# Performance work log

Hardware: AMD Instinct MI355X
Metric: run time of the kernel (lower is better)

The kernel has to match this reference:

```python
import jax, jax.numpy as jnp
import numpy as np

B, LQ, LK, E, H = 2, 1024, 10000, 256, 8
D = E // H  # head_dim = 32


def setup_inputs() -> dict:
    key = jax.random.key(0)
    ks = jax.random.split(key, 10)
    s = 1.0 / np.sqrt(E).astype(np.float32)
    return {
        "bev_emb": jax.random.normal(ks[0], (B, LK, E), jnp.float32),
        "queries": jax.random.normal(ks[1], (B, LQ, E), jnp.float32),
        "Wq": jax.random.normal(ks[2], (E, E), jnp.float32) * s,
        "bq": jax.random.normal(ks[3], (E,), jnp.float32) * 0.01,
        "Wk": jax.random.normal(ks[4], (E, E), jnp.float32) * s,
        "bk": jax.random.normal(ks[5], (E,), jnp.float32) * 0.01,
        "Wv": jax.random.normal(ks[6], (E, E), jnp.float32) * s,
        "bv": jax.random.normal(ks[7], (E,), jnp.float32) * 0.01,
        "Wo": jax.random.normal(ks[8], (E, E), jnp.float32) * s,
        "bo": jax.random.normal(ks[9], (E,), jnp.float32) * 0.01,
    }


def reference(bev_emb, queries, Wq, bq, Wk, bk, Wv, bv, Wo, bo):
    Bn, Lq, Em = queries.shape
    Lk = bev_emb.shape[1]
    q = (queries @ Wq + bq).reshape(Bn, Lq, H, D)
    k = (bev_emb @ Wk + bk).reshape(Bn, Lk, H, D)
    v = (bev_emb @ Wv + bv).reshape(Bn, Lk, H, D)
    # NOTE: source applies no 1/sqrt(head_dim) scaling
    energy = jnp.einsum('bqhd,bkhd->bhqk', q, k)  # [B,H,Lq,Lk]
    attn = jax.nn.softmax(energy, axis=-1)
    out = jnp.einsum('bhqk,bkhd->bqhd', attn, v).reshape(Bn, Lq, Em)
    return out @ Wo + bo
```

## Files before the change

### kernel.cpp

```cpp
#include <hip/hip_runtime.h>
#include <hip/hip_bf16.h>

#define B_  2
#define LQ_ 1024
#define LK_ 10000
#define E_  256
#define H_  8
#define D_  32
#define NT_ ((LK_ + 63) / 64)

typedef __attribute__((ext_vector_type(8))) short bf16x8;
typedef __attribute__((ext_vector_type(4))) short bf16x4;
typedef __attribute__((ext_vector_type(4))) float f32x4;

#define LOG2E 1.4426950408889634f

static __device__ __forceinline__ short bfc(float x) {
  __bf16 b = (__bf16)x;
  return __builtin_bit_cast(short, b);
}
static __device__ __forceinline__ float bf2f(short s) {
  return (float)__builtin_bit_cast(__bf16, s);
}

#if __has_builtin(__builtin_amdgcn_exp2f)
static __device__ __forceinline__ float ex2(float x) {
  return __builtin_amdgcn_exp2f(x);
}
#else
static __device__ __forceinline__ float ex2(float x) { return exp2f(x); }
#endif

#if __has_builtin(__builtin_amdgcn_mfma_f32_16x16x16bf16_1k)
static __device__ __forceinline__ f32x4 mfma_pv(bf16x4 a, bf16x4 b, f32x4 c) {
  return __builtin_amdgcn_mfma_f32_16x16x16bf16_1k(a, b, c, 0, 0, 0);
}
#else
static __device__ __forceinline__ f32x4 mfma_pv(bf16x4 a, bf16x4 b, f32x4 c) {
  asm volatile("s_nop 1\n\tv_mfma_f32_16x16x16_bf16 %0, %1, %2, %0"
               : "+v"(c) : "v"(a), "v"(b));
  return c;
}
#endif

static __device__ __forceinline__ int xcd_swizzle(int flat, int nwg) {
  const int xcd = flat & 7, rest = flat >> 3;
  const int q = nwg >> 3, r = nwg & 7;
  return (xcd < r ? xcd * (q + 1) : r * (q + 1) + (xcd - r) * q) + rest;
}

static __device__ __forceinline__ void split8(const float4& a, const float4& b,
                                              bf16x8& hi, bf16x8& lo) {
  float v[8] = {a.x, a.y, a.z, a.w, b.x, b.y, b.z, b.w};
#pragma unroll
  for (int i = 0; i < 8; ++i) {
    const short h = bfc(v[i]);
    hi[i] = h;
    lo[i] = bfc(v[i] - bf2f(h));
  }
}

__global__ __launch_bounds__(256) void wtrans4(
    const float* __restrict__ W0, const float* __restrict__ W1,
    const float* __restrict__ W2, const float* __restrict__ W3,
    unsigned short* __restrict__ T0, unsigned short* __restrict__ T1,
    unsigned short* __restrict__ T2, unsigned short* __restrict__ T3) {
  const float* W;
  unsigned short* T;
  switch (blockIdx.z) {
    case 0:  W = W0; T = T0; break;
    case 1:  W = W1; T = T1; break;
    case 2:  W = W2; T = T2; break;
    default: W = W3; T = T3; break;
  }
  __shared__ float ts[16][17];
  const int tx = threadIdx.x & 15;
  const int ty = threadIdx.x >> 4;
  const int k0 = blockIdx.x * 16;
  const int n0 = blockIdx.y * 16;
  ts[ty][tx] = W[(size_t)(k0 + ty) * 256 + n0 + tx];
  __syncthreads();
  T[(size_t)(n0 + ty) * 256 + k0 + tx] = (unsigned short)bfc(ts[tx][ty]);
}

template <bool KV, bool F32OUT>
__global__ __launch_bounds__(256) void proj_wave(
    const float* __restrict__ A,
    const unsigned short* __restrict__ Wt1,
    const unsigned short* __restrict__ Wt2,
    const float* __restrict__ b1, const float* __restrict__ b2,
    void* __restrict__ C1v, void* __restrict__ C2v) {
  const int lane = threadIdx.x & 63;
  const int nt   = threadIdx.x >> 6;
  const int mt   = blockIdx.x;
  const int lr   = lane & 15;
  const int oc   = lane >> 4;
  const int m0   = mt * 32;
  const int n0   = nt * 64;

  f32x4 ac1[2][4];
  f32x4 ac2[2][4];
#pragma unroll
  for (int s = 0; s < 2; ++s)
#pragma unroll
    for (int q = 0; q < 4; ++q) {
      ac1[s][q] = (f32x4){0.f, 0.f, 0.f, 0.f};
      if (KV) ac2[s][q] = (f32x4){0.f, 0.f, 0.f, 0.f};
    }

  const float* a0p = &A[(size_t)(m0 + lr) * 256 + oc * 8];
  const float* a1p = a0p + 16 * 256;

  float4 c0a = *(const float4*)(a0p + 0);
  float4 c0b = *(const float4*)(a0p + 4);
  float4 c1a = *(const float4*)(a1p + 0);
  float4 c1b = *(const float4*)(a1p + 4);

  for (int kb = 0; kb < 8; ++kb) {
    bf16x8 ah0, al0, ah1, al1;
    split8(c0a, c0b, ah0, al0);
    split8(c1a, c1b, ah1, al1);

    const size_t wko = (size_t)(kb * 32 + oc * 8);
    bf16x8 w1[4], w2[4];
#pragma unroll
    for (int q = 0; q < 4; ++q) {
      w1[q] = *(const bf16x8*)&Wt1[(size_t)(n0 + q * 16 + lr) * 256 + wko];
      if (KV) w2[q] = *(const bf16x8*)&Wt2[(size_t)(n0 + q * 16 + lr) * 256 + wko];
    }

    if (kb < 7) {
      c0a = *(const float4*)(a0p + (kb + 1) * 32 + 0);
      c0b = *(const float4*)(a0p + (kb + 1) * 32 + 4);
      c1a = *(const float4*)(a1p + (kb + 1) * 32 + 0);
      c1b = *(const float4*)(a1p + (kb + 1) * 32 + 4);
    }

#pragma unroll
    for (int q = 0; q < 4; ++q) {
      ac1[0][q] = __builtin_amdgcn_mfma_f32_16x16x32_bf16(w1[q], ah0, ac1[0][q], 0, 0, 0);
      ac1[0][q] = __builtin_amdgcn_mfma_f32_16x16x32_bf16(w1[q], al0, ac1[0][q], 0, 0, 0);
      ac1[1][q] = __builtin_amdgcn_mfma_f32_16x16x32_bf16(w1[q], ah1, ac1[1][q], 0, 0, 0);
      ac1[1][q] = __builtin_amdgcn_mfma_f32_16x16x32_bf16(w1[q], al1, ac1[1][q], 0, 0, 0);
      if (KV) {
        ac2[0][q] = __builtin_amdgcn_mfma_f32_16x16x32_bf16(w2[q], ah0, ac2[0][q], 0, 0, 0);
        ac2[1][q] = __builtin_amdgcn_mfma_f32_16x16x32_bf16(w2[q], ah1, ac2[1][q], 0, 0, 0);
      }
    }
  }

#pragma unroll
  for (int s = 0; s < 2; ++s) {
#pragma unroll
    for (int q = 0; q < 4; ++q) {
      const int m = m0 + s * 16 + lr;
      const int n = n0 + q * 16 + oc * 4;
      const float4 bv1 = *(const float4*)&b1[n];
      if (F32OUT) {
        float4 o;
        o.x = ac1[s][q][0] + bv1.x; o.y = ac1[s][q][1] + bv1.y;
        o.z = ac1[s][q][2] + bv1.z; o.w = ac1[s][q][3] + bv1.w;
        *(float4*)&((float*)C1v)[(size_t)m * 256 + n] = o;
      } else {
        ushort4 o;
        o.x = (unsigned short)bfc(ac1[s][q][0] + bv1.x);
        o.y = (unsigned short)bfc(ac1[s][q][1] + bv1.y);
        o.z = (unsigned short)bfc(ac1[s][q][2] + bv1.z);
        o.w = (unsigned short)bfc(ac1[s][q][3] + bv1.w);
        *(ushort4*)&((unsigned short*)C1v)[(size_t)m * 256 + n] = o;
      }
      if (KV) {
        const float4 bv2 = *(const float4*)&b2[n];
        ushort4 o;
        o.x = (unsigned short)bfc(ac2[s][q][0] + bv2.x);
        o.y = (unsigned short)bfc(ac2[s][q][1] + bv2.y);
        o.z = (unsigned short)bfc(ac2[s][q][2] + bv2.z);
        o.w = (unsigned short)bfc(ac2[s][q][3] + bv2.w);
        *(ushort4*)&((unsigned short*)C2v)[(size_t)m * 256 + n] = o;
      }
    }
  }
}

__global__ __launch_bounds__(256) void attn_mfma(const float* __restrict__ q,
                                                 const unsigned short* __restrict__ kbf,
                                                 const unsigned short* __restrict__ vbf,
                                                 float* __restrict__ Opart,
                                                 float* __restrict__ lpart,
                                                 float* __restrict__ o_direct,
                                                 int tiles_per_split, int nsplit) {
  const int nwg = 128 * gridDim.z;
  const int l   = xcd_swizzle(blockIdx.x + 16 * (blockIdx.y + 8 * blockIdx.z), nwg);
  const int qb   = l & 15;
  const int h    = (l >> 4) & 7;
  const int z    = l >> 7;
  const int s_id = z / B_;
  const int b    = z % B_;
  const int t    = threadIdx.x;
  const int lane = t & 63;
  const int w    = t >> 6;
  const int lq   = lane & 15;
  const int grp  = lane >> 4;

  __shared__ ushort Klds[2][64][64];
  __shared__ ushort Vtld[2][32][64];

  const int t0 = s_id * tiles_per_split;
  const int t1 = min(NT_, t0 + tiles_per_split);

  const int qrow = qb * 64 + w * 16 + lq;
  bf16x8 qfrag;
  {
    const float* qp = &q[((size_t)(b * LQ_ + qrow)) * E_ + h * D_ + grp * 8];
    const float4 q0 = *(const float4*)qp;
    const float4 q1 = *(const float4*)(qp + 4);
    qfrag[0] = bfc(q0.x * LOG2E); qfrag[1] = bfc(q0.y * LOG2E);
    qfrag[2] = bfc(q0.z * LOG2E); qfrag[3] = bfc(q0.w * LOG2E);
    qfrag[4] = bfc(q1.x * LOG2E); qfrag[5] = bfc(q1.y * LOG2E);
    qfrag[6] = bfc(q1.z * LOG2E); qfrag[7] = bfc(q1.w * LOG2E);
  }

  const int krow_l = t >> 2;
  const int kchunk = t & 3;
  const int vkp    = t >> 3;
  const int vd     = (t & 7) * 4;

  float l_run = 0.f;
  f32x4 acc0 = {0.f, 0.f, 0.f, 0.f};
  f32x4 acc1 = {0.f, 0.f, 0.f, 0.f};

  const size_t kvrow0 = (size_t)b * LK_;

  uint4 kval; ushort4 v0, v1;
  auto load_tile = [&](int kn) {
    if (kn == NT_ - 1) {
      const int krow  = min(kn * 64 + krow_l, LK_ - 1);
      const int vrow0 = min(kn * 64 + 2 * vkp, LK_ - 1);
      const int vrow1 = min(kn * 64 + 2 * vkp + 1, LK_ - 1);
      kval = *(const uint4*)&kbf[(kvrow0 + krow) * E_ + h * D_ + kchunk * 8];
      v0 = *(const ushort4*)&vbf[(kvrow0 + vrow0) * E_ + h * D_ + vd];
      v1 = *(const ushort4*)&vbf[(kvrow0 + vrow1) * E_ + h * D_ + vd];
    } else {
      kval = *(const uint4*)&kbf[(kvrow0 + kn * 64 + krow_l) * E_ + h * D_ + kchunk * 8];
      v0 = *(const ushort4*)&vbf[(kvrow0 + kn * 64 + 2 * vkp) * E_ + h * D_ + vd];
      v1 = *(const ushort4*)&vbf[(kvrow0 + kn * 64 + 2 * vkp + 1) * E_ + h * D_ + vd];
    }
  };
  auto store_tile = [&](int buf) {
    *(uint4*)((char*)&Klds[buf][krow_l][0] + ((kchunk * 16) ^ ((krow_l & 7) << 4))) = kval;
#pragma unroll
    for (int i = 0; i < 4; ++i) {
      const int d = vd + i;
      *(ushort2*)((char*)&Vtld[buf][d][0] + ((vkp * 4) ^ ((d & 7) << 4))) =
          make_ushort2(((const unsigned short*)&v0)[i], ((const unsigned short*)&v1)[i]);
    }
  };

  load_tile(t0);
  store_tile(0);
  if (t0 + 1 < t1) load_tile(t0 + 1);
  __syncthreads();

  int cur = 0;
  for (int kt = t0; kt < t1; ++kt) {
    const int rem = LK_ - kt * 64;

    if (kt + 1 < t1) store_tile(cur ^ 1);
    if (kt + 2 < t1) load_tile(kt + 2);

    f32x4 p[4];
    __builtin_amdgcn_s_setprio(1);
#pragma unroll
    for (int s = 0; s < 4; ++s) {
      const int row = s * 16 + lq;
      const bf16x8 kf = *(const bf16x8*)((const char*)&Klds[cur][row][0] +
                                         ((grp * 16) ^ ((row & 7) << 4)));
      const f32x4 zero = {0.f, 0.f, 0.f, 0.f};
      p[s] = __builtin_amdgcn_mfma_f32_16x16x32_bf16(kf, qfrag, zero, 0, 0, 0);
    }
    __builtin_amdgcn_s_setprio(0);

    bf16x4 pb[4];
    if (rem >= 64) {
#pragma unroll
      for (int s = 0; s < 4; ++s)
#pragma unroll
        for (int r = 0; r < 4; ++r) {
          const float e = ex2(p[s][r]);
          l_run += e;
          pb[s][r] = bfc(e);
        }
    } else {
#pragma unroll
      for (int s = 0; s < 4; ++s) {
        const bool vs = (s * 16 + grp * 4) < rem;
#pragma unroll
        for (int r = 0; r < 4; ++r) {
          const float e = vs ? ex2(p[s][r]) : 0.f;
          l_run += e;
          pb[s][r] = bfc(e);
        }
      }
    }

    __builtin_amdgcn_s_setprio(1);
#pragma unroll
    for (int s = 0; s < 4; ++s) {
      {
        const int row = lq;
        const bf16x4 vf = *(const bf16x4*)((const char*)&Vtld[cur][row][0] +
                                           ((s * 32 + grp * 8) ^ ((row & 7) << 4)));
        acc0 = mfma_pv(vf, pb[s], acc0);
      }
      {
        const int row = 16 + lq;
        const bf16x4 vf = *(const bf16x4*)((const char*)&Vtld[cur][row][0] +
                                           ((s * 32 + grp * 8) ^ ((row & 7) << 4)));
        acc1 = mfma_pv(vf, pb[s], acc1);
      }
    }
    __builtin_amdgcn_s_setprio(0);

    __syncthreads();
    cur ^= 1;
  }

  l_run += __shfl_xor(l_run, 16);
  l_run += __shfl_xor(l_run, 32);

  if (nsplit == 1) {
    const float inv = 1.f / l_run;
    float* op = &o_direct[((size_t)(b * LQ_ + qrow)) * E_ + h * D_];
#pragma unroll
    for (int r = 0; r < 4; ++r) {
      op[grp * 4 + r]      = acc0[r] * inv;
      op[16 + grp * 4 + r] = acc1[r] * inv;
    }
  } else {
    const size_t pbase =
        (size_t)s_id * (B_ * H_ * LQ_) + ((size_t)b * H_ + h) * LQ_ + qrow;
#pragma unroll
    for (int r = 0; r < 4; ++r) {
      Opart[pbase * D_ + grp * 4 + r]      = acc0[r];
      Opart[pbase * D_ + 16 + grp * 4 + r] = acc1[r];
    }
    if (grp == 0) lpart[pbase] = l_run;
  }
}

__global__ __launch_bounds__(256) void attn_merge(const float* __restrict__ Opart,
                                                  const float* __restrict__ lpart,
                                                  float* __restrict__ o, int S) {
  const int idx = blockIdx.x * 256 + threadIdx.x;
  if (idx >= B_ * LQ_ * E_) return;
  const int e   = idx & (E_ - 1);
  const int row = idx >> 8;
  const int b   = row >> 10;
  const int qq  = row & (LQ_ - 1);
  const int h   = e >> 5;
  const int d   = e & (D_ - 1);
  const size_t base   = ((size_t)b * H_ + h) * LQ_ + qq;
  const size_t stride = (size_t)B_ * H_ * LQ_;

  float lsum = 0.f, osum = 0.f;
  for (int s = 0; s < S; ++s) {
    lsum += lpart[s * stride + base];
    osum += Opart[(s * stride + base) * D_ + d];
  }
  o[idx] = osum / lsum;
}

extern "C" void kernel_launch(void* const* d_in, const int* in_sizes, int n_in,
                              void* d_out, int out_size, void* d_ws, size_t ws_size,
                              hipStream_t stream) {
  const float* bev     = (const float*)d_in[0];
  const float* queries = (const float*)d_in[1];
  const float* Wq      = (const float*)d_in[2];
  const float* bq      = (const float*)d_in[3];
  const float* Wk      = (const float*)d_in[4];
  const float* bk      = (const float*)d_in[5];
  const float* Wv      = (const float*)d_in[6];
  const float* bv      = (const float*)d_in[7];
  const float* Wo      = (const float*)d_in[8];
  const float* bo      = (const float*)d_in[9];
  float* out = (float*)d_out;

  const size_t nq = (size_t)B_ * LQ_ * E_;
  const size_t nk = (size_t)B_ * LK_ * E_;
  const size_t nw = (size_t)E_ * E_;
  float*          qws = (float*)d_ws;
  unsigned short* kbf = (unsigned short*)(qws + nq);
  unsigned short* vbf = kbf + nk;
  float*          ows = (float*)(vbf + nk);
  unsigned short* Wtq = (unsigned short*)(ows + nq);
  unsigned short* Wtk = Wtq + nw;
  unsigned short* Wtv = Wtk + nw;
  unsigned short* Wto = Wtv + nw;
  float*          opart = (float*)(Wto + nw);

  const size_t base_bytes = (nq * 2) * sizeof(float) +
                            (nk * 2 + nw * 4) * sizeof(unsigned short);
  const size_t per_split_bytes = (size_t)B_ * H_ * LQ_ * (D_ + 1) * sizeof(float);
  int S = 0;
  for (int cand = 8; cand >= 1; cand >>= 1) {
    if (base_bytes + (size_t)cand * per_split_bytes <= ws_size) { S = cand; break; }
  }

  wtrans4<<<dim3(16, 16, 4), 256, 0, stream>>>(Wq, Wk, Wv, Wo, Wtq, Wtk, Wtv, Wto);

  proj_wave<false, true><<<dim3(64), 256, 0, stream>>>(
      queries, Wtq, nullptr, bq, nullptr, qws, nullptr);
  proj_wave<true, false><<<dim3(625), 256, 0, stream>>>(
      bev, Wtk, Wtv, bk, bv, kbf, vbf);

  if (S <= 1) {
    attn_mfma<<<dim3(16, H_, B_), 256, 0, stream>>>(
        qws, kbf, vbf, nullptr, nullptr, ows, NT_, 1);
  } else {
    float* lpart = opart + (size_t)S * B_ * H_ * LQ_ * D_;
    const int tps = (NT_ + S - 1) / S;
    attn_mfma<<<dim3(16, H_, B_ * S), 256, 0, stream>>>(
        qws, kbf, vbf, opart, lpart, nullptr, tps, S);
    attn_merge<<<dim3((B_ * LQ_ * E_ + 255) / 256), 256, 0, stream>>>(
        opart, lpart, ows, S);
  }

  proj_wave<false, true><<<dim3(64), 256, 0, stream>>>(
      ows, Wto, nullptr, bo, nullptr, out, nullptr);
}
```

Before: 126.3 us.

## Process two query row groups per wave to reuse K/V tiles

Each wave now handles 32 query rows instead of 16, so a workgroup covers 128 query rows and reuses every K and V tile loaded into LDS for twice as many MFMAs. The grid's query-block dimension is halved to match. This cuts global K/V traffic and the LDS load/sync overhead per unit of work. In exchange it raises register pressure and halves the number of workgroups (to 64·B·S), which may reduce occupancy or leave CUs idle on a 256-CU part.

```diff
diff --git a/kernel.cpp b/kernel.cpp
--- a/kernel.cpp
+++ b/kernel.cpp
@@ -189,11 +189,11 @@
                                                  float* __restrict__ lpart,
                                                  float* __restrict__ o_direct,
                                                  int tiles_per_split, int nsplit) {
-  const int nwg = 128 * gridDim.z;
-  const int l   = xcd_swizzle(blockIdx.x + 16 * (blockIdx.y + 8 * blockIdx.z), nwg);
-  const int qb   = l & 15;
-  const int h    = (l >> 4) & 7;
-  const int z    = l >> 7;
+  const int nwg = 64 * gridDim.z;
+  const int l   = xcd_swizzle(blockIdx.x + 8 * (blockIdx.y + 8 * blockIdx.z), nwg);
+  const int qb   = l & 7;
+  const int h    = (l >> 3) & 7;
+  const int z    = l >> 6;
   const int s_id = z / B_;
   const int b    = z % B_;
   const int t    = threadIdx.x;
@@ -208,16 +208,24 @@
   const int t0 = s_id * tiles_per_split;
   const int t1 = min(NT_, t0 + tiles_per_split);
 
-  const int qrow = qb * 64 + w * 16 + lq;
-  bf16x8 qfrag;
+  const int qrowA = qb * 128 + w * 32 + lq;
+  const int qrowB = qrowA + 16;
+  bf16x8 qfA, qfB;
   {
-    const float* qp = &q[((size_t)(b * LQ_ + qrow)) * E_ + h * D_ + grp * 8];
-    const float4 q0 = *(const float4*)qp;
-    const float4 q1 = *(const float4*)(qp + 4);
-    qfrag[0] = bfc(q0.x * LOG2E); qfrag[1] = bfc(q0.y * LOG2E);
-    qfrag[2] = bfc(q0.z * LOG2E); qfrag[3] = bfc(q0.w * LOG2E);
-    qfrag[4] = bfc(q1.x * LOG2E); qfrag[5] = bfc(q1.y * LOG2E);
-    qfrag[6] = bfc(q1.z * LOG2E); qfrag[7] = bfc(q1.w * LOG2E);
+    const float* qpA = &q[((size_t)(b * LQ_ + qrowA)) * E_ + h * D_ + grp * 8];
+    const float* qpB = &q[((size_t)(b * LQ_ + qrowB)) * E_ + h * D_ + grp * 8];
+    const float4 a0 = *(const float4*)qpA;
+    const float4 a1 = *(const float4*)(qpA + 4);
+    const float4 b0 = *(const float4*)qpB;
+    const float4 b1 = *(const float4*)(qpB + 4);
+    qfA[0] = bfc(a0.x * LOG2E); qfA[1] = bfc(a0.y * LOG2E);
+    qfA[2] = bfc(a0.z * LOG2E); qfA[3] = bfc(a0.w * LOG2E);
+    qfA[4] = bfc(a1.x * LOG2E); qfA[5] = bfc(a1.y * LOG2E);
+    qfA[6] = bfc(a1.z * LOG2E); qfA[7] = bfc(a1.w * LOG2E);
+    qfB[0] = bfc(b0.x * LOG2E); qfB[1] = bfc(b0.y * LOG2E);
+    qfB[2] = bfc(b0.z * LOG2E); qfB[3] = bfc(b0.w * LOG2E);
+    qfB[4] = bfc(b1.x * LOG2E); qfB[5] = bfc(b1.y * LOG2E);
+    qfB[6] = bfc(b1.z * LOG2E); qfB[7] = bfc(b1.w * LOG2E);
   }
 
   const int krow_l = t >> 2;
@@ -225,9 +233,9 @@
   const int vkp    = t >> 3;
   const int vd     = (t & 7) * 4;
 
-  float l_run = 0.f;
-  f32x4 acc0 = {0.f, 0.f, 0.f, 0.f};
-  f32x4 acc1 = {0.f, 0.f, 0.f, 0.f};
+  float lA = 0.f, lB = 0.f;
+  f32x4 a0A = {0.f, 0.f, 0.f, 0.f}, a1A = {0.f, 0.f, 0.f, 0.f};
+  f32x4 a0B = {0.f, 0.f, 0.f, 0.f}, a1B = {0.f, 0.f, 0.f, 0.f};
 
   const size_t kvrow0 = (size_t)b * LK_;
 
@@ -268,7 +276,7 @@
     if (kt + 1 < t1) store_tile(cur ^ 1);
     if (kt + 2 < t1) load_tile(kt + 2);
 
-    f32x4 p[4];
+    f32x4 pA[4], pB[4];
     __builtin_amdgcn_s_setprio(1);
 #pragma unroll
     for (int s = 0; s < 4; ++s) {
@@ -276,19 +284,21 @@
       const bf16x8 kf = *(const bf16x8*)((const char*)&Klds[cur][row][0] +
                                          ((grp * 16) ^ ((row & 7) << 4)));
       const f32x4 zero = {0.f, 0.f, 0.f, 0.f};
-      p[s] = __builtin_amdgcn_mfma_f32_16x16x32_bf16(kf, qfrag, zero, 0, 0, 0);
+      pA[s] = __builtin_amdgcn_mfma_f32_16x16x32_bf16(kf, qfA, zero, 0, 0, 0);
+      pB[s] = __builtin_amdgcn_mfma_f32_16x16x32_bf16(kf, qfB, zero, 0, 0, 0);
     }
     __builtin_amdgcn_s_setprio(0);
 
-    bf16x4 pb[4];
+    bf16x4 pbA[4], pbB[4];
     if (rem >= 64) {
 #pragma unroll
       for (int s = 0; s < 4; ++s)
 #pragma unroll
         for (int r = 0; r < 4; ++r) {
-          const float e = ex2(p[s][r]);
-          l_run += e;
-          pb[s][r] = bfc(e);
+          const float eA = ex2(pA[s][r]);
+          const float eB = ex2(pB[s][r]);
+          lA += eA; lB += eB;
+          pbA[s][r] = bfc(eA); pbB[s][r] = bfc(eB);
         }
     } else {
 #pragma unroll
@@ -296,9 +306,10 @@
         const bool vs = (s * 16 + grp * 4) < rem;
 #pragma unroll
         for (int r = 0; r < 4; ++r) {
-          const float e = vs ? ex2(p[s][r]) : 0.f;
-          l_run += e;
-          pb[s][r] = bfc(e);
+          const float eA = vs ? ex2(pA[s][r]) : 0.f;
+          const float eB = vs ? ex2(pB[s][r]) : 0.f;
+          lA += eA; lB += eB;
+          pbA[s][r] = bfc(eA); pbB[s][r] = bfc(eB);
         }
       }
     }
@@ -310,13 +321,15 @@
         const int row = lq;
         const bf16x4 vf = *(const bf16x4*)((const char*)&Vtld[cur][row][0] +
                                            ((s * 32 + grp * 8) ^ ((row & 7) << 4)));
-        acc0 = mfma_pv(vf, pb[s], acc0);
+        a0A = mfma_pv(vf, pbA[s], a0A);
+        a0B = mfma_pv(vf, pbB[s], a0B);
       }
       {
         const int row = 16 + lq;
         const bf16x4 vf = *(const bf16x4*)((const char*)&Vtld[cur][row][0] +
                                            ((s * 32 + grp * 8) ^ ((row & 7) << 4)));
-        acc1 = mfma_pv(vf, pb[s], acc1);
+        a1A = mfma_pv(vf, pbA[s], a1A);
+        a1B = mfma_pv(vf, pbB[s], a1B);
       }
     }
     __builtin_amdgcn_s_setprio(0);
@@ -325,26 +338,38 @@
     cur ^= 1;
   }
 
-  l_run += __shfl_xor(l_run, 16);
-  l_run += __shfl_xor(l_run, 32);
+  lA += __shfl_xor(lA, 16);
+  lA += __shfl_xor(lA, 32);
+  lB += __shfl_xor(lB, 16);
+  lB += __shfl_xor(lB, 32);
 
   if (nsplit == 1) {
-    const float inv = 1.f / l_run;
-    float* op = &o_direct[((size_t)(b * LQ_ + qrow)) * E_ + h * D_];
+    const float invA = 1.f / lA;
+    const float invB = 1.f / lB;
+    float* opA = &o_direct[((size_t)(b * LQ_ + qrowA)) * E_ + h * D_];
+    float* opB = &o_direct[((size_t)(b * LQ_ + qrowB)) * E_ + h * D_];
 #pragma unroll
     for (int r = 0; r < 4; ++r) {
-      op[grp * 4 + r]      = acc0[r] * inv;
-      op[16 + grp * 4 + r] = acc1[r] * inv;
+      opA[grp * 4 + r]      = a0A[r] * invA;
+      opA[16 + grp * 4 + r] = a1A[r] * invA;
+      opB[grp * 4 + r]      = a0B[r] * invB;
+      opB[16 + grp * 4 + r] = a1B[r] * invB;
     }
   } else {
-    const size_t pbase =
-        (size_t)s_id * (B_ * H_ * LQ_) + ((size_t)b * H_ + h) * LQ_ + qrow;
+    const size_t pbA =
+        (size_t)s_id * (B_ * H_ * LQ_) + ((size_t)b * H_ + h) * LQ_ + qrowA;
+    const size_t pbB = pbA + 16;
 #pragma unroll
     for (int r = 0; r < 4; ++r) {
-      Opart[pbase * D_ + grp * 4 + r]      = acc0[r];
-      Opart[pbase * D_ + 16 + grp * 4 + r] = acc1[r];
-    }
-    if (grp == 0) lpart[pbase] = l_run;
+      Opart[pbA * D_ + grp * 4 + r]      = a0A[r];
+      Opart[pbA * D_ + 16 + grp * 4 + r] = a1A[r];
+      Opart[pbB * D_ + grp * 4 + r]      = a0B[r];
+      Opart[pbB * D_ + 16 + grp * 4 + r] = a1B[r];
+    }
+    if (grp == 0) {
+      lpart[pbA] = lA;
+      lpart[pbB] = lB;
+    }
   }
 }
 
@@ -414,12 +439,12 @@
       bev, Wtk, Wtv, bk, bv, kbf, vbf);
 
   if (S <= 1) {
-    attn_mfma<<<dim3(16, H_, B_), 256, 0, stream>>>(
+    attn_mfma<<<dim3(8, H_, B_), 256, 0, stream>>>(
         qws, kbf, vbf, nullptr, nullptr, ows, NT_, 1);
   } else {
     float* lpart = opart + (size_t)S * B_ * H_ * LQ_ * D_;
     const int tps = (NT_ + S - 1) / S;
-    attn_mfma<<<dim3(16, H_, B_ * S), 256, 0, stream>>>(
+    attn_mfma<<<dim3(8, H_, B_ * S), 256, 0, stream>>>(
         qws, kbf, vbf, opart, lpart, nullptr, tps, S);
     attn_merge<<<dim3((B_ * LQ_ * E_ + 255) / 256), 256, 0, stream>>>(
         opart, lpart, ows, S);
```

After: 128.4 us. About the same (+1.7%).
